# Performance work log

Measured on AMD Instinct MI355X. Metric: run time of the kernel, lower is better.

## Reference

```python
import jax, jax.numpy as jnp
import numpy as np

N_NODES = 65536
N_EDGES = 1048576
IN_CH, HID_CH, OUT_CH = 300, 64, 20
DROPOUT_P = 0.5


def setup_inputs() -> dict:
    key = jax.random.key(0)
    ks = jax.random.split(key, 6)
    x = jax.random.normal(ks[0], (N_NODES, IN_CH), dtype=jnp.float32)
    edge_index = jax.random.randint(ks[1], (2, N_EDGES), 0, N_NODES, dtype=jnp.int64)
    edge_weight = jax.random.uniform(ks[2], (N_EDGES,), dtype=jnp.float32)
    # Glorot-ish init for linear weights (PyG lin has no bias; GCNConv adds its own bias)
    W1 = jax.random.normal(ks[3], (IN_CH, HID_CH), dtype=jnp.float32) / np.sqrt(IN_CH)
    b1 = jnp.zeros((HID_CH,), dtype=jnp.float32)
    W2 = jax.random.normal(ks[4], (HID_CH, OUT_CH), dtype=jnp.float32) / np.sqrt(HID_CH)
    b2 = jnp.zeros((OUT_CH,), dtype=jnp.float32)
    return {"x": x, "edge_index": edge_index, "edge_weight": edge_weight,
            "W1": W1, "b1": b1, "W2": W2, "b2": b2}


def _gcn_conv(x, src, dst, edge_weight, W, b, num_nodes):
    # GCNConv with add_self_loops=False, normalize=False:
    #   h = x @ W; out[i] = sum_{e: dst(e)=i} w_e * h[src(e)]; out += b
    h = x @ W                                   # [N, C_out]
    msg = h[src] * edge_weight[:, None]         # [E, C_out]
    agg = jax.ops.segment_sum(msg, dst, num_segments=num_nodes)
    return agg + b


def reference(x, edge_index, edge_weight, W1, b1, W2, b2):
    num_nodes = x.shape[0]
    src, dst = edge_index[0], edge_index[1]
    h = _gcn_conv(x, src, dst, edge_weight, W1, b1, num_nodes)
    h = jax.nn.relu(h)
    # dropout p=0.5, training=True, deterministic fixed key
    keep = jax.random.bernoulli(jax.random.key(42), 1.0 - DROPOUT_P, h.shape)
    h = jnp.where(keep, h / (1.0 - DROPOUT_P), 0.0)
    out = _gcn_conv(h, src, dst, edge_weight, W2, b2, num_nodes)
    return out
```

## Files before the change

kernel.cpp:

```cpp
#include <hip/hip_runtime.h>

#define N_NODES 65536
#define N_EDGES 1048576
#define NB 256
#define CAP 4608
#define EPB_A 4096
#define BLK_A (N_EDGES / EPB_A)
#define EPT_A (EPB_A / 1024)
#define WT_BLK 20
#define GEMM_BLK (N_NODES / 64)

typedef __attribute__((ext_vector_type(8))) short short8v;
typedef __attribute__((ext_vector_type(4))) float float4v;

__device__ __forceinline__ unsigned short f2bf(float f) {
  unsigned u = __float_as_uint(f);
  unsigned r = u + 0x7FFFu + ((u >> 16) & 1u);
  return (unsigned short)(r >> 16);
}
__device__ __forceinline__ float bflo(unsigned u) { return __uint_as_float(u << 16); }
__device__ __forceinline__ float bfhi(unsigned u) { return __uint_as_float(u & 0xFFFF0000u); }

__device__ __forceinline__ bool keep_mask(unsigned idx) {
  const unsigned k0 = 0u, k1 = 42u;
  const unsigned k2 = 0x1BD11BDAu ^ k0 ^ k1;
  unsigned x0 = 0u;
  unsigned x1 = idx;
  x0 += k0; x1 += k1;
#define TF_ROUND(r) { x0 += x1; x1 = (x1 << (r)) | (x1 >> (32 - (r))); x1 ^= x0; }
  TF_ROUND(13) TF_ROUND(15) TF_ROUND(26) TF_ROUND(6)
  x0 += k1; x1 += k2 + 1u;
  TF_ROUND(17) TF_ROUND(29) TF_ROUND(16) TF_ROUND(24)
  x0 += k2; x1 += k0 + 2u;
  TF_ROUND(13) TF_ROUND(15) TF_ROUND(26) TF_ROUND(6)
  x0 += k0; x1 += k1 + 3u;
  TF_ROUND(17) TF_ROUND(29) TF_ROUND(16) TF_ROUND(24)
  x0 += k1; x1 += k2 + 4u;
  TF_ROUND(13) TF_ROUND(15) TF_ROUND(26) TF_ROUND(6)
  x0 += k2; x1 += k0 + 5u;
#undef TF_ROUND
  return ((x0 ^ x1) & 0x80000000u) == 0u;
}

__global__ __launch_bounds__(1024) void binpass2(const int* __restrict__ ei,
                                                 const float* __restrict__ ew,
                                                 const float* __restrict__ W1,
                                                 uint2* __restrict__ binned2,
                                                 unsigned* __restrict__ cnt_mat,
                                                 unsigned* __restrict__ lofs_mat,
                                                 unsigned short* __restrict__ Wt) {
  const int b = blockIdx.x;
  const int t = threadIdx.x;
  if (b >= BLK_A) {
    int i = (b - BLK_A) * 1024 + t;
    int ch = i / 320, k = i % 320;
    Wt[i] = f2bf((k < 300) ? W1[k * 64 + ch] : 0.0f);
    return;
  }
  __shared__ unsigned cnt[NB], lofs[NB], lcur[NB];
  __shared__ uint2 stage[EPB_A];
  const int e0 = b * EPB_A;
  if (t < NB) { cnt[t] = 0u; lcur[t] = 0u; }
  __syncthreads();
  unsigned pk[EPT_A], pw[EPT_A];
#pragma unroll
  for (int j = 0; j < EPT_A; ++j) {
    int e = e0 + t + j * 1024;
    unsigned s = (unsigned)ei[e];
    unsigned d = (unsigned)ei[N_EDGES + e];
    pk[j] = s | (d << 16);
    pw[j] = __float_as_uint(ew[e]);
    atomicAdd(&cnt[d >> 8], 1u);
  }
  __syncthreads();
  if (t < NB) lofs[t] = cnt[t];
  __syncthreads();
  for (int d = 1; d < NB; d <<= 1) {
    unsigned u = 0u;
    if (t < NB && t >= d) u = lofs[t - d];
    __syncthreads();
    if (t < NB) lofs[t] += u;
    __syncthreads();
  }
  if (t < NB) {
    lofs[t] -= cnt[t];
    cnt_mat[(unsigned)b * NB + t]  = cnt[t];
    lofs_mat[(unsigned)b * NB + t] = lofs[t];
  }
  __syncthreads();
#pragma unroll
  for (int j = 0; j < EPT_A; ++j) {
    unsigned bk = pk[j] >> 24;
    unsigned slot = lofs[bk] + atomicAdd(&lcur[bk], 1u);
    stage[slot] = make_uint2(pk[j], pw[j]);
  }
  __syncthreads();
  uint2* dst = binned2 + (size_t)b * EPB_A;
  for (int s = t; s < EPB_A; s += 1024) dst[s] = stage[s];
}

__device__ __forceinline__ void bucket_body2(unsigned char* raw, int b,
                                             const unsigned* __restrict__ cnt_mat,
                                             const unsigned* __restrict__ lofs_mat,
                                             const uint2* __restrict__ binned2,
                                             unsigned* __restrict__ sortedc,
                                             unsigned* __restrict__ offs_p) {
  uint2*    eLDS    = (uint2*)raw;
  unsigned* scnt_s  = (unsigned*)(raw + 36864);
  unsigned* sbase_s = scnt_s + NB;
  unsigned* mst_s   = sbase_s + NB;
  unsigned* cnt     = mst_s + NB;
  unsigned* cur     = cnt + NB;
  unsigned* tot     = cur + NB;
  const int t = threadIdx.x;
  const unsigned scnt = cnt_mat[(unsigned)t * NB + b];
  const unsigned sofs = lofs_mat[(unsigned)t * NB + b];
  scnt_s[t]  = scnt;
  sbase_s[t] = (unsigned)t * EPB_A + sofs;
  cnt[t] = 0u;
  cur[t] = scnt;
  __syncthreads();
  for (int d = 1; d < NB; d <<= 1) {
    unsigned u = (t >= d) ? cur[t - d] : 0u;
    __syncthreads();
    cur[t] += u;
    __syncthreads();
  }
  mst_s[t] = cur[t] - scnt;
  if (t == NB - 1) *tot = cur[t];
  __syncthreads();
  const unsigned n_edges = *tot;
  const int g = t >> 4, j0 = t & 15;
  for (int seg = g; seg < NB; seg += 16) {
    const unsigned sc = scnt_s[seg];
    const unsigned sb = sbase_s[seg];
    const unsigned ms = mst_s[seg];
    for (unsigned j = (unsigned)j0; j < sc; j += 16)
      eLDS[ms + j] = binned2[sb + j];
  }
  __syncthreads();
  for (unsigned i = t; i < n_edges; i += 256)
    atomicAdd(&cnt[(eLDS[i].x >> 16) & 255u], 1u);
  __syncthreads();
  cur[t] = cnt[t];
  __syncthreads();
  for (int d = 1; d < NB; d <<= 1) {
    unsigned u = (t >= d) ? cur[t - d] : 0u;
    __syncthreads();
    cur[t] += u;
    __syncthreads();
  }
  const unsigned lo = (unsigned)b * CAP;
  unsigned excl = cur[t] - cnt[t];
  offs_p[b * NB + t] = (lo + excl) | (cnt[t] << 21);
  __syncthreads();
  cur[t] = excl;
  __syncthreads();
  for (unsigned i = t; i < n_edges; i += 256) {
    uint2 u = eLDS[i];
    unsigned lo8 = (u.x >> 16) & 255u;
    unsigned p = lo + atomicAdd(&cur[lo8], 1u);
    sortedc[p] = (u.x & 0xFFFFu) | ((unsigned)f2bf(__uint_as_float(u.y)) << 16);
  }
}

__device__ __forceinline__ void gemm1_body(unsigned char* smraw, int nb,
                                           const float* __restrict__ x,
                                           const unsigned short* __restrict__ Wt,
                                           unsigned short* __restrict__ h1b) {
  unsigned short (*As)[72] = (unsigned short (*)[72])smraw;
  unsigned short (*Bs)[72] = (unsigned short (*)[72])(smraw + 9216);
  const int t = threadIdx.x;
  const int node0 = nb * 64;
  const int wave = t >> 6, lane = t & 63;
  const int quad = lane >> 4, l16 = lane & 15;
  float4v acc[4] = {{0.f,0.f,0.f,0.f},{0.f,0.f,0.f,0.f},{0.f,0.f,0.f,0.f},{0.f,0.f,0.f,0.f}};

  for (int kt = 0; kt < 5; ++kt) {
    const int k0 = kt * 64;
    for (int f = t; f < 1024; f += 256) {
      int node = f >> 4;
      int k = (f & 15) * 4;
      uint2 packed;
      if (k0 + k < 300) {
        float4 v = *(const float4*)(x + (size_t)(node0 + node) * 300 + k0 + k);
        packed.x = (unsigned)f2bf(v.x) | ((unsigned)f2bf(v.y) << 16);
        packed.y = (unsigned)f2bf(v.z) | ((unsigned)f2bf(v.w) << 16);
      } else {
        packed.x = 0u; packed.y = 0u;
      }
      *(uint2*)&As[node][k] = packed;
    }
    for (int f = t; f < 512; f += 256) {
      int ch = f >> 3;
      int kq = f & 7;
      uint4 v = *(const uint4*)(Wt + (size_t)ch * 320 + k0 + kq * 8);
      *(uint4*)&Bs[ch][kq * 8] = v;
    }
    __syncthreads();
    short8v a0 = *(const short8v*)&As[wave * 16 + l16][quad * 8];
    short8v a1 = *(const short8v*)&As[wave * 16 + l16][32 + quad * 8];
#pragma unroll
    for (int nt = 0; nt < 4; ++nt) {
      short8v b0 = *(const short8v*)&Bs[nt * 16 + l16][quad * 8];
      short8v b1 = *(const short8v*)&Bs[nt * 16 + l16][32 + quad * 8];
      acc[nt] = __builtin_amdgcn_mfma_f32_16x16x32_bf16(a0, b0, acc[nt], 0, 0, 0);
      acc[nt] = __builtin_amdgcn_mfma_f32_16x16x32_bf16(a1, b1, acc[nt], 0, 0, 0);
    }
    __syncthreads();
  }
#pragma unroll
  for (int nt = 0; nt < 4; ++nt) {
#pragma unroll
    for (int r = 0; r < 4; ++r) {
      h1b[(size_t)(node0 + wave * 16 + quad * 4 + r) * 64 + nt * 16 + l16] = f2bf(acc[nt][r]);
    }
  }
}

__global__ __launch_bounds__(256) void bucketsort_gemm1(const unsigned* __restrict__ cnt_mat,
                                                        const unsigned* __restrict__ lofs_mat,
                                                        const uint2* __restrict__ binned2,
                                                        unsigned* __restrict__ sortedc,
                                                        unsigned* __restrict__ offs_p,
                                                        const float* __restrict__ x,
                                                        const unsigned short* __restrict__ Wt,
                                                        unsigned short* __restrict__ h1b) {
  __shared__ __align__(16) unsigned char sm[41988];
  if (blockIdx.x < NB) {
    bucket_body2(sm, blockIdx.x, cnt_mat, lofs_mat, binned2, sortedc, offs_p);
  } else {
    gemm1_body(sm, blockIdx.x - NB, x, Wt, h1b);
  }
}

__global__ __launch_bounds__(256) void agg1_gemm2(const unsigned* __restrict__ offs_p,
                                                  const unsigned* __restrict__ sortedc,
                                                  const unsigned short* __restrict__ h1b,
                                                  const float* __restrict__ b1,
                                                  const float* __restrict__ W2,
                                                  unsigned* __restrict__ g32u) {
  __shared__ float h2[16][68];
  __shared__ float w2t[20][68];
  const int t = threadIdx.x;
  const int node0 = blockIdx.x * 16;
  for (int i = t; i < 20 * 64; i += 256) {
    int row = i >> 6, col = i & 63;
    w2t[row][col] = W2[col * 20 + row];
  }
  const int n = t >> 4, cg = t & 15;
  const int node = node0 + n;
  const unsigned op = offs_p[node];
  const unsigned s = op & 0x1FFFFFu;
  const unsigned e_end = s + (op >> 21);
  float4 acc = *(const float4*)(b1 + cg * 4);
  unsigned i = s;
  for (; i + 8 <= e_end; i += 8) {
    unsigned e0 = sortedc[i],     e1 = sortedc[i + 1], e2 = sortedc[i + 2], e3 = sortedc[i + 3];
    unsigned e4 = sortedc[i + 4], e5 = sortedc[i + 5], e6 = sortedc[i + 6], e7 = sortedc[i + 7];
    uint2 v0 = *(const uint2*)(h1b + ((size_t)(e0 & 0xFFFFu)) * 64 + cg * 4);
    uint2 v1 = *(const uint2*)(h1b + ((size_t)(e1 & 0xFFFFu)) * 64 + cg * 4);
    uint2 v2 = *(const uint2*)(h1b + ((size_t)(e2 & 0xFFFFu)) * 64 + cg * 4);
    uint2 v3 = *(const uint2*)(h1b + ((size_t)(e3 & 0xFFFFu)) * 64 + cg * 4);
    uint2 v4 = *(const uint2*)(h1b + ((size_t)(e4 & 0xFFFFu)) * 64 + cg * 4);
    uint2 v5 = *(const uint2*)(h1b + ((size_t)(e5 & 0xFFFFu)) * 64 + cg * 4);
    uint2 v6 = *(const uint2*)(h1b + ((size_t)(e6 & 0xFFFFu)) * 64 + cg * 4);
    uint2 v7 = *(const uint2*)(h1b + ((size_t)(e7 & 0xFFFFu)) * 64 + cg * 4);
    float w0 = bfhi(e0), w1 = bfhi(e1), w2 = bfhi(e2), w3 = bfhi(e3);
    float w4 = bfhi(e4), w5 = bfhi(e5), w6 = bfhi(e6), w7 = bfhi(e7);
    acc.x = fmaf(w0, bflo(v0.x), acc.x); acc.y = fmaf(w0, bfhi(v0.x), acc.y);
    acc.z = fmaf(w0, bflo(v0.y), acc.z); acc.w = fmaf(w0, bfhi(v0.y), acc.w);
    acc.x = fmaf(w1, bflo(v1.x), acc.x); acc.y = fmaf(w1, bfhi(v1.x), acc.y);
    acc.z = fmaf(w1, bflo(v1.y), acc.z); acc.w = fmaf(w1, bfhi(v1.y), acc.w);
    acc.x = fmaf(w2, bflo(v2.x), acc.x); acc.y = fmaf(w2, bfhi(v2.x), acc.y);
    acc.z = fmaf(w2, bflo(v2.y), acc.z); acc.w = fmaf(w2, bfhi(v2.y), acc.w);
    acc.x = fmaf(w3, bflo(v3.x), acc.x); acc.y = fmaf(w3, bfhi(v3.x), acc.y);
    acc.z = fmaf(w3, bflo(v3.y), acc.z); acc.w = fmaf(w3, bfhi(v3.y), acc.w);
    acc.x = fmaf(w4, bflo(v4.x), acc.x); acc.y = fmaf(w4, bfhi(v4.x), acc.y);
    acc.z = fmaf(w4, bflo(v4.y), acc.z); acc.w = fmaf(w4, bfhi(v4.y), acc.w);
    acc.x = fmaf(w5, bflo(v5.x), acc.x); acc.y = fmaf(w5, bfhi(v5.x), acc.y);
    acc.z = fmaf(w5, bflo(v5.y), acc.z); acc.w = fmaf(w5, bfhi(v5.y), acc.w);
    acc.x = fmaf(w6, bflo(v6.x), acc.x); acc.y = fmaf(w6, bfhi(v6.x), acc.y);
    acc.z = fmaf(w6, bflo(v6.y), acc.z); acc.w = fmaf(w6, bfhi(v6.y), acc.w);
    acc.x = fmaf(w7, bflo(v7.x), acc.x); acc.y = fmaf(w7, bfhi(v7.x), acc.y);
    acc.z = fmaf(w7, bflo(v7.y), acc.z); acc.w = fmaf(w7, bfhi(v7.y), acc.w);
  }
  for (; i < e_end; ++i) {
    unsigned e0 = sortedc[i];
    uint2 v0 = *(const uint2*)(h1b + ((size_t)(e0 & 0xFFFFu)) * 64 + cg * 4);
    float w0 = bfhi(e0);
    acc.x = fmaf(w0, bflo(v0.x), acc.x); acc.y = fmaf(w0, bfhi(v0.x), acc.y);
    acc.z = fmaf(w0, bflo(v0.y), acc.z); acc.w = fmaf(w0, bfhi(v0.y), acc.w);
  }
  const unsigned gi = (unsigned)node * 64u + (unsigned)cg * 4u;
  float r[4] = {acc.x, acc.y, acc.z, acc.w};
#pragma unroll
  for (int j = 0; j < 4; ++j) {
    float v = fmaxf(r[j], 0.0f);
    h2[n][cg * 4 + j] = keep_mask(gi + j) ? v * 2.0f : 0.0f;
  }
  __syncthreads();
  float d0 = 0.0f, d1 = 0.0f;
  if (cg < 10) {
    const int c0 = cg * 2, c1 = cg * 2 + 1;
#pragma unroll
    for (int k = 0; k < 64; k += 4) {
      float4 hv = *(const float4*)(&h2[n][k]);
      float4 w0 = *(const float4*)(&w2t[c0][k]);
      float4 w1 = *(const float4*)(&w2t[c1][k]);
      d0 = fmaf(hv.x, w0.x, d0); d0 = fmaf(hv.y, w0.y, d0);
      d0 = fmaf(hv.z, w0.z, d0); d0 = fmaf(hv.w, w0.w, d0);
      d1 = fmaf(hv.x, w1.x, d1); d1 = fmaf(hv.y, w1.y, d1);
      d1 = fmaf(hv.z, w1.z, d1); d1 = fmaf(hv.w, w1.w, d1);
    }
  }
  unsigned packed = (cg < 10) ? ((unsigned)f2bf(d0) | ((unsigned)f2bf(d1) << 16)) : 0u;
  g32u[(size_t)node * 16 + cg] = packed;
}

__global__ __launch_bounds__(256) void aggregate2(const unsigned* __restrict__ offs_p,
                                                  const unsigned* __restrict__ sortedc,
                                                  const unsigned* __restrict__ g32u,
                                                  const float* __restrict__ b2,
                                                  float* __restrict__ out) {
  const int t = threadIdx.x;
  const int n = blockIdx.x * 16 + (t >> 4);
  const int cg = t & 15;
  const unsigned op = offs_p[n];
  const unsigned s = op & 0x1FFFFFu;
  const unsigned e_end = s + (op >> 21);
  float ax = 0.0f, ay = 0.0f;
  unsigned i = s;
  for (; i + 8 <= e_end; i += 8) {
    unsigned e0 = sortedc[i],     e1 = sortedc[i + 1], e2 = sortedc[i + 2], e3 = sortedc[i + 3];
    unsigned e4 = sortedc[i + 4], e5 = sortedc[i + 5], e6 = sortedc[i + 6], e7 = sortedc[i + 7];
    unsigned v0 = g32u[(size_t)(e0 & 0xFFFFu) * 16 + cg];
    unsigned v1 = g32u[(size_t)(e1 & 0xFFFFu) * 16 + cg];
    unsigned v2 = g32u[(size_t)(e2 & 0xFFFFu) * 16 + cg];
    unsigned v3 = g32u[(size_t)(e3 & 0xFFFFu) * 16 + cg];
    unsigned v4 = g32u[(size_t)(e4 & 0xFFFFu) * 16 + cg];
    unsigned v5 = g32u[(size_t)(e5 & 0xFFFFu) * 16 + cg];
    unsigned v6 = g32u[(size_t)(e6 & 0xFFFFu) * 16 + cg];
    unsigned v7 = g32u[(size_t)(e7 & 0xFFFFu) * 16 + cg];
    float w0 = bfhi(e0), w1 = bfhi(e1), w2 = bfhi(e2), w3 = bfhi(e3);
    float w4 = bfhi(e4), w5 = bfhi(e5), w6 = bfhi(e6), w7 = bfhi(e7);
    ax = fmaf(w0, bflo(v0), ax); ay = fmaf(w0, bfhi(v0), ay);
    ax = fmaf(w1, bflo(v1), ax); ay = fmaf(w1, bfhi(v1), ay);
    ax = fmaf(w2, bflo(v2), ax); ay = fmaf(w2, bfhi(v2), ay);
    ax = fmaf(w3, bflo(v3), ax); ay = fmaf(w3, bfhi(v3), ay);
    ax = fmaf(w4, bflo(v4), ax); ay = fmaf(w4, bfhi(v4), ay);
    ax = fmaf(w5, bflo(v5), ax); ay = fmaf(w5, bfhi(v5), ay);
    ax = fmaf(w6, bflo(v6), ax); ay = fmaf(w6, bfhi(v6), ay);
    ax = fmaf(w7, bflo(v7), ax); ay = fmaf(w7, bfhi(v7), ay);
  }
  for (; i < e_end; ++i) {
    unsigned e0 = sortedc[i];
    unsigned v0 = g32u[(size_t)(e0 & 0xFFFFu) * 16 + cg];
    float w0 = bfhi(e0);
    ax = fmaf(w0, bflo(v0), ax); ay = fmaf(w0, bfhi(v0), ay);
  }
  if (cg < 10) {
    float2 o = make_float2(ax + b2[cg * 2], ay + b2[cg * 2 + 1]);
    *(float2*)(out + (size_t)n * 20 + cg * 2) = o;
  }
}

extern "C" void kernel_launch(void* const* d_in, const int* in_sizes, int n_in,
                              void* d_out, int out_size, void* d_ws, size_t ws_size,
                              hipStream_t stream) {
  const float* x  = (const float*)d_in[0];
  const int*   ei = (const int*)d_in[1];
  const float* ew = (const float*)d_in[2];
  const float* W1 = (const float*)d_in[3];
  const float* b1 = (const float*)d_in[4];
  const float* W2 = (const float*)d_in[5];
  const float* b2 = (const float*)d_in[6];
  float* out = (float*)d_out;

  unsigned short* h1b      = (unsigned short*)d_ws;
  unsigned*       g32u     = (unsigned*)(h1b + (size_t)N_NODES * 64);
  uint2*          binned2  = (uint2*)(g32u + (size_t)N_NODES * 16);
  unsigned*       sortedc  = (unsigned*)(binned2 + (size_t)N_EDGES);
  unsigned*       offs_p   = sortedc + (size_t)NB * CAP;
  unsigned*       cnt_mat  = offs_p + N_NODES;
  unsigned*       lofs_mat = cnt_mat + (size_t)BLK_A * NB;
  unsigned short* Wt       = (unsigned short*)(lofs_mat + (size_t)BLK_A * NB);

  binpass2<<<BLK_A + WT_BLK, 1024, 0, stream>>>(ei, ew, W1, binned2, cnt_mat, lofs_mat, Wt);
  bucketsort_gemm1<<<NB + GEMM_BLK, 256, 0, stream>>>(cnt_mat, lofs_mat, binned2,
                                                      sortedc, offs_p, x, Wt, h1b);
  agg1_gemm2<<<N_NODES / 16, 256, 0, stream>>>(offs_p, sortedc, h1b, b1, W2, g32u);
  aggregate2<<<N_NODES / 16, 256, 0, stream>>>(offs_p, sortedc, g32u, b2, out);
}
```

Baseline: 222.0 us.

## Split binned edges into packed value array and byte key array

```diff
diff --git a/kernel.cpp b/kernel.cpp
--- a/kernel.cpp
+++ b/kernel.cpp
@@ -45,7 +45,8 @@
 __global__ __launch_bounds__(1024) void binpass2(const int* __restrict__ ei,
                                                  const float* __restrict__ ew,
                                                  const float* __restrict__ W1,
-                                                 uint2* __restrict__ binned2,
+                                                 unsigned* __restrict__ val2,
+                                                 unsigned char* __restrict__ key2,
                                                  unsigned* __restrict__ cnt_mat,
                                                  unsigned* __restrict__ lofs_mat,
                                                  unsigned short* __restrict__ Wt) {
@@ -58,19 +59,21 @@
     return;
   }
   __shared__ unsigned cnt[NB], lofs[NB], lcur[NB];
-  __shared__ uint2 stage[EPB_A];
+  __shared__ unsigned stage_val[EPB_A];
+  __shared__ unsigned char stage_key[EPB_A];
   const int e0 = b * EPB_A;
   if (t < NB) { cnt[t] = 0u; lcur[t] = 0u; }
   __syncthreads();
-  unsigned pk[EPT_A], pw[EPT_A];
+  unsigned pv[EPT_A], pb[EPT_A], pk8[EPT_A];
 #pragma unroll
   for (int j = 0; j < EPT_A; ++j) {
     int e = e0 + t + j * 1024;
     unsigned s = (unsigned)ei[e];
     unsigned d = (unsigned)ei[N_EDGES + e];
-    pk[j] = s | (d << 16);
-    pw[j] = __float_as_uint(ew[e]);
-    atomicAdd(&cnt[d >> 8], 1u);
+    pv[j]  = s | ((unsigned)f2bf(ew[e]) << 16);
+    pb[j]  = d >> 8;
+    pk8[j] = d & 255u;
+    atomicAdd(&cnt[pb[j]], 1u);
   }
   __syncthreads();
   if (t < NB) lofs[t] = cnt[t];
@@ -90,28 +93,30 @@
   __syncthreads();
 #pragma unroll
   for (int j = 0; j < EPT_A; ++j) {
-    unsigned bk = pk[j] >> 24;
+    unsigned bk = pb[j];
     unsigned slot = lofs[bk] + atomicAdd(&lcur[bk], 1u);
-    stage[slot] = make_uint2(pk[j], pw[j]);
-  }
-  __syncthreads();
-  uint2* dst = binned2 + (size_t)b * EPB_A;
-  for (int s = t; s < EPB_A; s += 1024) dst[s] = stage[s];
-}
-
-__device__ __forceinline__ void bucket_body2(unsigned char* raw, int b,
+    stage_val[slot] = pv[j];
+    stage_key[slot] = (unsigned char)pk8[j];
+  }
+  __syncthreads();
+  unsigned* dv = val2 + (size_t)b * EPB_A;
+  unsigned char* dk = key2 + (size_t)b * EPB_A;
+  for (int s = t; s < EPB_A; s += 1024) { dv[s] = stage_val[s]; dk[s] = stage_key[s]; }
+}
+
+__device__ __forceinline__ void bucket_body3(unsigned char* raw, int b,
                                              const unsigned* __restrict__ cnt_mat,
                                              const unsigned* __restrict__ lofs_mat,
-                                             const uint2* __restrict__ binned2,
+                                             const unsigned* __restrict__ val2,
+                                             const unsigned char* __restrict__ key2,
                                              unsigned* __restrict__ sortedc,
                                              unsigned* __restrict__ offs_p) {
-  uint2*    eLDS    = (uint2*)raw;
-  unsigned* scnt_s  = (unsigned*)(raw + 36864);
+  unsigned char* kLDS   = raw;
+  unsigned* scnt_s  = (unsigned*)(raw + 4608);
   unsigned* sbase_s = scnt_s + NB;
   unsigned* mst_s   = sbase_s + NB;
   unsigned* cnt     = mst_s + NB;
   unsigned* cur     = cnt + NB;
-  unsigned* tot     = cur + NB;
   const int t = threadIdx.x;
   const unsigned scnt = cnt_mat[(unsigned)t * NB + b];
   const unsigned sofs = lofs_mat[(unsigned)t * NB + b];
@@ -127,22 +132,22 @@
     __syncthreads();
   }
   mst_s[t] = cur[t] - scnt;
-  if (t == NB - 1) *tot = cur[t];
-  __syncthreads();
-  const unsigned n_edges = *tot;
+  __syncthreads();
+  const unsigned n_edges = cur[NB - 1];
   const int g = t >> 4, j0 = t & 15;
   for (int seg = g; seg < NB; seg += 16) {
     const unsigned sc = scnt_s[seg];
     const unsigned sb = sbase_s[seg];
     const unsigned ms = mst_s[seg];
     for (unsigned j = (unsigned)j0; j < sc; j += 16)
-      eLDS[ms + j] = binned2[sb + j];
+      kLDS[ms + j] = key2[sb + j];
   }
   __syncthreads();
   for (unsigned i = t; i < n_edges; i += 256)
-    atomicAdd(&cnt[(eLDS[i].x >> 16) & 255u], 1u);
-  __syncthreads();
-  cur[t] = cnt[t];
+    atomicAdd(&cnt[kLDS[i]], 1u);
+  __syncthreads();
+  const unsigned myc = cnt[t];
+  cur[t] = myc;
   __syncthreads();
   for (int d = 1; d < NB; d <<= 1) {
     unsigned u = (t >= d) ? cur[t - d] : 0u;
@@ -151,16 +156,21 @@
     __syncthreads();
   }
   const unsigned lo = (unsigned)b * CAP;
-  unsigned excl = cur[t] - cnt[t];
-  offs_p[b * NB + t] = (lo + excl) | (cnt[t] << 21);
+  unsigned excl = cur[t] - myc;
+  offs_p[b * NB + t] = (lo + excl) | (myc << 21);
   __syncthreads();
   cur[t] = excl;
   __syncthreads();
-  for (unsigned i = t; i < n_edges; i += 256) {
-    uint2 u = eLDS[i];
-    unsigned lo8 = (u.x >> 16) & 255u;
-    unsigned p = lo + atomicAdd(&cur[lo8], 1u);
-    sortedc[p] = (u.x & 0xFFFFu) | ((unsigned)f2bf(__uint_as_float(u.y)) << 16);
+  for (int seg = g; seg < NB; seg += 16) {
+    const unsigned sc = scnt_s[seg];
+    const unsigned sb = sbase_s[seg];
+    const unsigned ms = mst_s[seg];
+    for (unsigned j = (unsigned)j0; j < sc; j += 16) {
+      unsigned v = val2[sb + j];
+      unsigned k = kLDS[ms + j];
+      unsigned p = lo + atomicAdd(&cur[k], 1u);
+      sortedc[p] = v;
+    }
   }
 }
 
@@ -220,15 +230,16 @@
 
 __global__ __launch_bounds__(256) void bucketsort_gemm1(const unsigned* __restrict__ cnt_mat,
                                                         const unsigned* __restrict__ lofs_mat,
-                                                        const uint2* __restrict__ binned2,
+                                                        const unsigned* __restrict__ val2,
+                                                        const unsigned char* __restrict__ key2,
                                                         unsigned* __restrict__ sortedc,
                                                         unsigned* __restrict__ offs_p,
                                                         const float* __restrict__ x,
                                                         const unsigned short* __restrict__ Wt,
                                                         unsigned short* __restrict__ h1b) {
-  __shared__ __align__(16) unsigned char sm[41988];
+  __shared__ __align__(16) unsigned char sm[18432];
   if (blockIdx.x < NB) {
-    bucket_body2(sm, blockIdx.x, cnt_mat, lofs_mat, binned2, sortedc, offs_p);
+    bucket_body3(sm, blockIdx.x, cnt_mat, lofs_mat, val2, key2, sortedc, offs_p);
   } else {
     gemm1_body(sm, blockIdx.x - NB, x, Wt, h1b);
   }
@@ -379,15 +390,16 @@
 
   unsigned short* h1b      = (unsigned short*)d_ws;
   unsigned*       g32u     = (unsigned*)(h1b + (size_t)N_NODES * 64);
-  uint2*          binned2  = (uint2*)(g32u + (size_t)N_NODES * 16);
-  unsigned*       sortedc  = (unsigned*)(binned2 + (size_t)N_EDGES);
+  unsigned*       val2     = g32u + (size_t)N_NODES * 16;
+  unsigned*       sortedc  = val2 + (size_t)N_EDGES;
   unsigned*       offs_p   = sortedc + (size_t)NB * CAP;
   unsigned*       cnt_mat  = offs_p + N_NODES;
   unsigned*       lofs_mat = cnt_mat + (size_t)BLK_A * NB;
-  unsigned short* Wt       = (unsigned short*)(lofs_mat + (size_t)BLK_A * NB);
-
-  binpass2<<<BLK_A + WT_BLK, 1024, 0, stream>>>(ei, ew, W1, binned2, cnt_mat, lofs_mat, Wt);
-  bucketsort_gemm1<<<NB + GEMM_BLK, 256, 0, stream>>>(cnt_mat, lofs_mat, binned2,
+  unsigned char*  key2     = (unsigned char*)(lofs_mat + (size_t)BLK_A * NB);
+  unsigned short* Wt       = (unsigned short*)(key2 + (size_t)N_EDGES);
+
+  binpass2<<<BLK_A + WT_BLK, 1024, 0, stream>>>(ei, ew, W1, val2, key2, cnt_mat, lofs_mat, Wt);
+  bucketsort_gemm1<<<NB + GEMM_BLK, 256, 0, stream>>>(cnt_mat, lofs_mat, val2, key2,
                                                       sortedc, offs_p, x, Wt, h1b);
   agg1_gemm2<<<N_NODES / 16, 256, 0, stream>>>(offs_p, sortedc, h1b, b1, W2, g32u);
   aggregate2<<<N_NODES / 16, 256, 0, stream>>>(offs_p, sortedc, g32u, b2, out);
```

New measurement: 212.2 us. -4.4%, faster.
